# Kernel optimization log

Measured on AMD Instinct MI355X. Metric: run time of the kernel, lower is better.

Reference implementation:

```python
import jax, jax.numpy as jnp
import numpy as np

B, S, D, H, FF = 4, 1024, 1024, 16, 4096
DH = D // H
EPS = 1e-5


def setup_inputs() -> dict:
    key = jax.random.key(0)
    ks = jax.random.split(key, 24)
    w = lambda i, shp: jax.random.normal(ks[i], shp, jnp.float32) * 0.02
    inp = {
        'tgt': jax.random.normal(ks[0], (B, S, D), jnp.float32),
        'memory': jax.random.normal(ks[1], (B, S, D), jnp.float32),
        'mask': jax.random.randint(ks[2], (B, S, S), 0, 2, jnp.int32),
        # self-attention projections (stored [in,out]; torch Linear weight transposed)
        'sa_wq': w(3, (D, D)), 'sa_bq': jnp.zeros((D,), jnp.float32),
        'sa_wk': w(4, (D, D)), 'sa_bk': jnp.zeros((D,), jnp.float32),
        'sa_wv': w(5, (D, D)), 'sa_bv': jnp.zeros((D,), jnp.float32),
        'sa_wo': w(6, (D, D)), 'sa_bo': jnp.zeros((D,), jnp.float32),
        # cross-attention projections
        'ca_wq': w(7, (D, D)), 'ca_bq': jnp.zeros((D,), jnp.float32),
        'ca_wk': w(8, (D, D)), 'ca_bk': jnp.zeros((D,), jnp.float32),
        'ca_wv': w(9, (D, D)), 'ca_bv': jnp.zeros((D,), jnp.float32),
        'ca_wo': w(10, (D, D)), 'ca_bo': jnp.zeros((D,), jnp.float32),
        # FFN
        'w1': w(11, (D, FF)), 'b1': jnp.zeros((FF,), jnp.float32),
        'w2': w(12, (FF, D)), 'b2': jnp.zeros((D,), jnp.float32),
        # LayerNorms
        'g1': jnp.ones((D,), jnp.float32), 'be1': jnp.zeros((D,), jnp.float32),
        'g2': jnp.ones((D,), jnp.float32), 'be2': jnp.zeros((D,), jnp.float32),
        'g3': jnp.ones((D,), jnp.float32), 'be3': jnp.zeros((D,), jnp.float32),
    }
    return inp


def _layernorm(x, g, b):
    m = jnp.mean(x, axis=-1, keepdims=True)
    v = jnp.mean((x - m) ** 2, axis=-1, keepdims=True)
    return (x - m) * jax.lax.rsqrt(v + EPS) * g + b


def _mha(x, y, mask, wq, bq, wk, bk, wv, bv, wo, bo):
    # chunk(h,-1)+cat(0) head-split == reshape to [B,S,H,DH]
    b_, sq, _ = x.shape
    sk = y.shape[1]
    q = (x @ wq + bq).reshape(b_, sq, H, DH)
    k = (y @ wk + bk).reshape(b_, sk, H, DH)
    v = (y @ wv + bv).reshape(b_, sk, H, DH)
    score = jnp.einsum('bqhd,bkhd->bhqk', q, k) / jnp.float32(np.sqrt(DH))
    score = score + (1.0 - mask[:, None].astype(score.dtype)) * (-1e9)
    attn = jax.nn.softmax(score, axis=-1)
    out = jnp.einsum('bhqk,bkhd->bqhd', attn, v).reshape(b_, sq, D)
    return out @ wo + bo


def reference(tgt, memory, mask,
              sa_wq, sa_bq, sa_wk, sa_bk, sa_wv, sa_bv, sa_wo, sa_bo,
              ca_wq, ca_bq, ca_wk, ca_bk, ca_wv, ca_bv, ca_wo, ca_bo,
              w1, b1, w2, b2, g1, be1, g2, be2, g3, be3):
    t = tgt + _mha(tgt, tgt, mask, sa_wq, sa_bq, sa_wk, sa_bk, sa_wv, sa_bv, sa_wo, sa_bo)
    t = _layernorm(t, g1, be1)
    t = t + _mha(t, memory, mask, ca_wq, ca_bq, ca_wk, ca_bk, ca_wv, ca_bv, ca_wo, ca_bo)
    t = _layernorm(t, g2, be2)
    t = t + (jax.nn.relu(t @ w1 + b1) @ w2 + b2)
    t = _layernorm(t, g3, be3)
    return t
```

## Files before the change

kernel.cpp:

```cpp
#include <hip/hip_runtime.h>
#include <math.h>

typedef float f32x4 __attribute__((ext_vector_type(4)));
typedef unsigned short ushort8 __attribute__((ext_vector_type(8)));
typedef unsigned short ushort4v __attribute__((ext_vector_type(4)));
typedef __bf16 bf16x8 __attribute__((ext_vector_type(8)));
typedef unsigned int u32;

__device__ __forceinline__ unsigned short f2bf(float x) {
  union { float f; unsigned u; } v; v.f = x;
  unsigned r = v.u + 0x7FFFu + ((v.u >> 16) & 1u);
  return (unsigned short)(r >> 16);
}

__device__ __forceinline__ f32x4 mfma16(ushort8 a, ushort8 b, f32x4 c) {
  return __builtin_amdgcn_mfma_f32_16x16x32_bf16(
      __builtin_bit_cast(bf16x8, a), __builtin_bit_cast(bf16x8, b), c, 0, 0, 0);
}

__device__ __forceinline__ void gload16(const void* g, void* l) {
  __builtin_amdgcn_global_load_lds((const __attribute__((address_space(1))) u32*)g,
                                   (__attribute__((address_space(3))) u32*)l, 16, 0, 0);
}

__global__ __launch_bounds__(256) void gemm_bf16_kernel(
    const unsigned short* __restrict__ A, const unsigned short* __restrict__ Bt,
    const float* __restrict__ bias, void* __restrict__ C,
    int M, int N, int K, int flags)
{
  __shared__ __align__(16) char As0[128 * 128];
  __shared__ __align__(16) char Bs0[128 * 128];
  __shared__ __align__(16) char As1[128 * 128];
  __shared__ __align__(16) char Bs1[128 * 128];
  const int bn = blockIdx.x, bm = blockIdx.y;
  const int t = threadIdx.x;
  const int lane = t & 63, w = t >> 6, wm = w >> 1, wn = w & 1;
  const int l4 = lane & 15, lg = lane >> 4;
  const size_t K2 = (size_t)K * 2;

  f32x4 acc[4][4];
#pragma unroll
  for (int i = 0; i < 4; ++i)
#pragma unroll
    for (int j = 0; j < 4; ++j) acc[i][j] = f32x4{0.f, 0.f, 0.f, 0.f};

  const int lr = lane >> 3;
  const int ls = (lane & 7) ^ lr;
  const char* Ag = (const char*)A + (size_t)(bm * 128 + w * 32 + lr) * K2 + ls * 16;
  const char* Bg = (const char*)Bt + (size_t)(bn * 128 + w * 32 + lr) * K2 + ls * 16;
  const int wo = w * 4096;

  auto STAGE = [&](char* Al, char* Bl, int kt) {
    const size_t ko = (size_t)kt * 128;
#pragma unroll
    for (int i = 0; i < 4; ++i) {
      gload16(Ag + i * 8 * K2 + ko, Al + wo + i * 1024);
      gload16(Bg + i * 8 * K2 + ko, Bl + wo + i * 1024);
    }
  };
  auto COMPUTE = [&](const char* As, const char* Bs) {
#pragma unroll
    for (int ks = 0; ks < 2; ++ks) {
      const int kb = ks * 64 + lg * 16;
      ushort8 af[4], bfr[4];
#pragma unroll
      for (int mi = 0; mi < 4; ++mi) {
        int r = wm * 64 + mi * 16 + l4;
        af[mi] = *reinterpret_cast<const ushort8*>(As + r * 128 + (kb ^ ((r & 7) << 4)));
      }
#pragma unroll
      for (int ni = 0; ni < 4; ++ni) {
        int r = wn * 64 + ni * 16 + l4;
        bfr[ni] = *reinterpret_cast<const ushort8*>(Bs + r * 128 + (kb ^ ((r & 7) << 4)));
      }
#pragma unroll
      for (int mi = 0; mi < 4; ++mi)
#pragma unroll
        for (int ni = 0; ni < 4; ++ni)
          acc[mi][ni] = mfma16(af[mi], bfr[ni], acc[mi][ni]);
    }
  };

  const int nkt = K >> 6;
  STAGE(As0, Bs0, 0);
  __syncthreads();
  for (int kt = 0; kt < nkt; kt += 2) {
    STAGE(As1, Bs1, kt + 1);
    COMPUTE(As0, Bs0);
    __syncthreads();
    if (kt + 2 < nkt) STAGE(As0, Bs0, kt + 2);
    COMPUTE(As1, Bs1);
    __syncthreads();
  }

  const int relu = flags & 1, obf = flags & 2;
#pragma unroll
  for (int mi = 0; mi < 4; ++mi)
#pragma unroll
    for (int ni = 0; ni < 4; ++ni) {
      int col = bn * 128 + wn * 64 + ni * 16 + l4;
      float bia = bias[col];
#pragma unroll
      for (int j = 0; j < 4; ++j) {
        int row = bm * 128 + wm * 64 + mi * 16 + lg * 4 + j;
        float vv = acc[mi][ni][j] + bia;
        if (relu) vv = fmaxf(vv, 0.f);
        if (obf) ((unsigned short*)C)[(size_t)row * N + col] = f2bf(vv);
        else     ((float*)C)[(size_t)row * N + col] = vv;
      }
    }
}

constexpr int kS = 1024, kD = 1024, kDH = 64;

__global__ __launch_bounds__(256) void attn_kernel(
    const unsigned short* __restrict__ Qg, const unsigned short* __restrict__ Kg,
    const unsigned short* __restrict__ Vg, int qs, int ks_,
    const int* __restrict__ maskg, unsigned short* __restrict__ Og)
{
  __shared__ __align__(16) char Qs[64 * 128];
  __shared__ __align__(16) char Ks[64 * 128];
  __shared__ __align__(16) char VTs[64 * 128];
  __shared__ __align__(16) char Ps[4 * 16 * 128];
  const int qt = blockIdx.x, h = blockIdx.y, b = blockIdx.z;
  const int t = threadIdx.x, lane = t & 63, w = t >> 6;
  const int l4 = lane & 15, lg = lane >> 4;

  {
    int r = t >> 2, c0 = (t & 3) * 16;
    const unsigned short* src = Qg + (size_t)(b * kS + qt * 64 + r) * qs + h * kDH + c0;
#pragma unroll
    for (int hf = 0; hf < 2; ++hf) {
      ushort8 v = *reinterpret_cast<const ushort8*>(src + hf * 8);
      int c = c0 + hf * 8;
      *reinterpret_cast<ushort8*>(Qs + r * 128 + ((c * 2) ^ ((r & 7) << 4))) = v;
    }
  }

  float m_r[4], l_r[4];
  f32x4 o[4];
#pragma unroll
  for (int j = 0; j < 4; ++j) { m_r[j] = -1e30f; l_r[j] = 0.f; }
#pragma unroll
  for (int di = 0; di < 4; ++di) o[di] = f32x4{0.f, 0.f, 0.f, 0.f};

  for (int kt = 0; kt < kS / 64; ++kt) {
    __syncthreads();
    {
      int r = t >> 2, c0 = (t & 3) * 16;
      const unsigned short* src = Kg + (size_t)(b * kS + kt * 64 + r) * ks_ + h * kDH + c0;
#pragma unroll
      for (int hf = 0; hf < 2; ++hf) {
        ushort8 v = *reinterpret_cast<const ushort8*>(src + hf * 8);
        int c = c0 + hf * 8;
        *reinterpret_cast<ushort8*>(Ks + r * 128 + ((c * 2) ^ ((r & 7) << 4))) = v;
      }
    }
    {
      int key = t >> 2, c0 = (t & 3) * 16;
      const unsigned short* src = Vg + (size_t)(b * kS + kt * 64 + key) * ks_ + h * kDH + c0;
      ushort8 v0 = *reinterpret_cast<const ushort8*>(src);
      ushort8 v1 = *reinterpret_cast<const ushort8*>(src + 8);
#pragma unroll
      for (int i = 0; i < 16; ++i) {
        int dh = c0 + i;
        unsigned short vv = (i < 8) ? v0[i] : v1[i - 8];
        *reinterpret_cast<unsigned short*>(VTs + dh * 128 + ((key * 2) ^ ((dh & 7) << 4))) = vv;
      }
    }
    __syncthreads();

    f32x4 sc[4];
#pragma unroll
    for (int ni = 0; ni < 4; ++ni) sc[ni] = f32x4{0.f, 0.f, 0.f, 0.f};
#pragma unroll
    for (int ks = 0; ks < 2; ++ks) {
      const int kb = ks * 64 + lg * 16;
      int qr = w * 16 + l4;
      ushort8 a = *reinterpret_cast<const ushort8*>(Qs + qr * 128 + (kb ^ ((qr & 7) << 4)));
#pragma unroll
      for (int ni = 0; ni < 4; ++ni) {
        int kr = ni * 16 + l4;
        ushort8 bb = *reinterpret_cast<const ushort8*>(Ks + kr * 128 + (kb ^ ((kr & 7) << 4)));
        sc[ni] = mfma16(a, bb, sc[ni]);
      }
    }

    const int qbase = qt * 64 + w * 16;
    float pmax[4];
#pragma unroll
    for (int j = 0; j < 4; ++j) {
      int qrow = qbase + lg * 4 + j;
      const int* mrow = maskg + ((size_t)b * kS + qrow) * kS + kt * 64;
#pragma unroll
      for (int ni = 0; ni < 4; ++ni) {
        float mv = (float)mrow[ni * 16 + l4];
        sc[ni][j] = sc[ni][j] * 0.125f + (1.0f - mv) * (-1e9f);
      }
      pmax[j] = fmaxf(fmaxf(sc[0][j], sc[1][j]), fmaxf(sc[2][j], sc[3][j]));
    }
#pragma unroll
    for (int j = 0; j < 4; ++j)
#pragma unroll
      for (int off = 1; off < 16; off <<= 1)
        pmax[j] = fmaxf(pmax[j], __shfl_xor(pmax[j], off, 64));
    float alpha[4], rsum[4];
#pragma unroll
    for (int j = 0; j < 4; ++j) {
      float mn = fmaxf(m_r[j], pmax[j]);
      alpha[j] = __expf(m_r[j] - mn);
      m_r[j] = mn;
      rsum[j] = 0.f;
    }
#pragma unroll
    for (int ni = 0; ni < 4; ++ni)
#pragma unroll
      for (int j = 0; j < 4; ++j) {
        float p = __expf(sc[ni][j] - m_r[j]);
        sc[ni][j] = p;
        rsum[j] += p;
      }
#pragma unroll
    for (int j = 0; j < 4; ++j) {
#pragma unroll
      for (int off = 1; off < 16; off <<= 1)
        rsum[j] += __shfl_xor(rsum[j], off, 64);
      l_r[j] = l_r[j] * alpha[j] + rsum[j];
    }
#pragma unroll
    for (int di = 0; di < 4; ++di)
#pragma unroll
      for (int j = 0; j < 4; ++j) o[di][j] *= alpha[j];

    {
      char* Pw = Ps + w * 2048;
#pragma unroll
      for (int ni = 0; ni < 4; ++ni)
#pragma unroll
        for (int j = 0; j < 4; ++j) {
          int row = lg * 4 + j, col = ni * 16 + l4;
          *reinterpret_cast<unsigned short*>(Pw + row * 128 + ((col * 2) ^ ((row & 7) << 4))) = f2bf(sc[ni][j]);
        }
    }
    __syncthreads();
    {
      const char* Pw = Ps + w * 2048;
#pragma unroll
      for (int ks = 0; ks < 2; ++ks) {
        const int kb = ks * 64 + lg * 16;
        ushort8 pa = *reinterpret_cast<const ushort8*>(Pw + l4 * 128 + (kb ^ ((l4 & 7) << 4)));
#pragma unroll
        for (int di = 0; di < 4; ++di) {
          int vr = di * 16 + l4;
          ushort8 vb = *reinterpret_cast<const ushort8*>(VTs + vr * 128 + (kb ^ ((vr & 7) << 4)));
          o[di] = mfma16(pa, vb, o[di]);
        }
      }
    }
  }

#pragma unroll
  for (int di = 0; di < 4; ++di) {
    int col = h * kDH + di * 16 + l4;
#pragma unroll
    for (int j = 0; j < 4; ++j) {
      int qrow = qt * 64 + w * 16 + lg * 4 + j;
      Og[(size_t)(b * kS + qrow) * kD + col] = f2bf(o[di][j] / l_r[j]);
    }
  }
}

__global__ __launch_bounds__(256) void addln_kernel(
    const float* __restrict__ x, const float* __restrict__ y,
    const float* __restrict__ g, const float* __restrict__ be,
    float* __restrict__ out, unsigned short* __restrict__ ob)
{
  const int row = blockIdx.x, t = threadIdx.x;
  const size_t base = (size_t)row * 1024 + t * 4;
  float4 xv = *reinterpret_cast<const float4*>(x + base);
  float4 yv = *reinterpret_cast<const float4*>(y + base);
  float v0 = xv.x + yv.x, v1 = xv.y + yv.y, v2 = xv.z + yv.z, v3 = xv.w + yv.w;
  float s1 = v0 + v1 + v2 + v3;
  float s2 = v0 * v0 + v1 * v1 + v2 * v2 + v3 * v3;
#pragma unroll
  for (int off = 1; off < 64; off <<= 1) {
    s1 += __shfl_xor(s1, off, 64);
    s2 += __shfl_xor(s2, off, 64);
  }
  __shared__ float r1[4], r2[4];
  const int w = t >> 6, lane = t & 63;
  if (lane == 0) { r1[w] = s1; r2[w] = s2; }
  __syncthreads();
  s1 = r1[0] + r1[1] + r1[2] + r1[3];
  s2 = r2[0] + r2[1] + r2[2] + r2[3];
  const float mean = s1 * (1.0f / 1024.0f);
  const float var = s2 * (1.0f / 1024.0f) - mean * mean;
  const float rs = rsqrtf(var + 1e-5f);
  float4 gv = *reinterpret_cast<const float4*>(g + t * 4);
  float4 bv = *reinterpret_cast<const float4*>(be + t * 4);
  float4 ov;
  ov.x = (v0 - mean) * rs * gv.x + bv.x;
  ov.y = (v1 - mean) * rs * gv.y + bv.y;
  ov.z = (v2 - mean) * rs * gv.z + bv.z;
  ov.w = (v3 - mean) * rs * gv.w + bv.w;
  *reinterpret_cast<float4*>(out + base) = ov;
  if (ob) {
    ushort4v bo;
    bo[0] = f2bf(ov.x); bo[1] = f2bf(ov.y); bo[2] = f2bf(ov.z); bo[3] = f2bf(ov.w);
    *reinterpret_cast<ushort4v*>(ob + base) = bo;
  }
}

__global__ __launch_bounds__(256) void cvt2_bf16_kernel(
    const float* __restrict__ a, const float* __restrict__ b,
    unsigned short* __restrict__ da, unsigned short* __restrict__ db, int n8each)
{
  int i = blockIdx.x * 256 + threadIdx.x;
  const float* s = a; unsigned short* d = da;
  if (i >= n8each) { s = b; d = db; i -= n8each; }
  if (i >= n8each) return;
  float4 f0 = reinterpret_cast<const float4*>(s)[i * 2];
  float4 f1 = reinterpret_cast<const float4*>(s)[i * 2 + 1];
  ushort8 v;
  v[0] = f2bf(f0.x); v[1] = f2bf(f0.y); v[2] = f2bf(f0.z); v[3] = f2bf(f0.w);
  v[4] = f2bf(f1.x); v[5] = f2bf(f1.y); v[6] = f2bf(f1.z); v[7] = f2bf(f1.w);
  reinterpret_cast<ushort8*>(d)[i] = v;
}

__global__ __launch_bounds__(256) void transpose_cvt_kernel(
    const float* __restrict__ src, unsigned short* __restrict__ dst, int K, int N)
{
  __shared__ float tile[32][33];
  const int bx = blockIdx.x, by = blockIdx.y;
  const int tx = threadIdx.x & 31, ty = threadIdx.x >> 5;
#pragma unroll
  for (int i = 0; i < 4; ++i)
    tile[ty + i * 8][tx] = src[(size_t)(by * 32 + ty + i * 8) * N + bx * 32 + tx];
  __syncthreads();
#pragma unroll
  for (int i = 0; i < 4; ++i)
    dst[(size_t)(bx * 32 + ty + i * 8) * K + by * 32 + tx] = f2bf(tile[tx][ty + i * 8]);
}

struct TPtrs { const float* s[8]; unsigned short* d[8]; };
__global__ __launch_bounds__(256) void tcvt_batch_kernel(TPtrs p)
{
  __shared__ float tile[32][33];
  const float* __restrict__ src = p.s[blockIdx.z];
  unsigned short* __restrict__ dst = p.d[blockIdx.z];
  const int bx = blockIdx.x, by = blockIdx.y;
  const int tx = threadIdx.x & 31, ty = threadIdx.x >> 5;
#pragma unroll
  for (int i = 0; i < 4; ++i)
    tile[ty + i * 8][tx] = src[(size_t)(by * 32 + ty + i * 8) * 1024 + bx * 32 + tx];
  __syncthreads();
#pragma unroll
  for (int i = 0; i < 4; ++i)
    dst[(size_t)(bx * 32 + ty + i * 8) * 1024 + by * 32 + tx] = f2bf(tile[tx][ty + i * 8]);
}

__global__ void biasprep_kernel(const float* sq, const float* sk, const float* sv,
                                const float* ck, const float* cv,
                                float* bsa, float* bca)
{
  int i = blockIdx.x * 256 + threadIdx.x;
  if (i < 3072) bsa[i] = (i < 1024) ? sq[i] : (i < 2048 ? sk[i - 1024] : sv[i - 2048]);
  int j = i - 3072;
  if (j >= 0 && j < 2048) bca[j] = (j < 1024) ? ck[j] : cv[j - 1024];
}

extern "C" void kernel_launch(void* const* d_in, const int* in_sizes, int n_in,
                              void* d_out, int out_size, void* d_ws, size_t ws_size,
                              hipStream_t stream)
{
  const float* tgt  = (const float*)d_in[0];
  const float* memi = (const float*)d_in[1];
  const int*   mask = (const int*)d_in[2];
  const float* sa_wq = (const float*)d_in[3];  const float* sa_bq = (const float*)d_in[4];
  const float* sa_wk = (const float*)d_in[5];  const float* sa_bk = (const float*)d_in[6];
  const float* sa_wv = (const float*)d_in[7];  const float* sa_bv = (const float*)d_in[8];
  const float* sa_wo = (const float*)d_in[9];  const float* sa_bo = (const float*)d_in[10];
  const float* ca_wq = (const float*)d_in[11]; const float* ca_bq = (const float*)d_in[12];
  const float* ca_wk = (const float*)d_in[13]; const float* ca_bk = (const float*)d_in[14];
  const float* ca_wv = (const float*)d_in[15]; const float* ca_bv = (const float*)d_in[16];
  const float* ca_wo = (const float*)d_in[17]; const float* ca_bo = (const float*)d_in[18];
  const float* w1 = (const float*)d_in[19]; const float* b1 = (const float*)d_in[20];
  const float* w2 = (const float*)d_in[21]; const float* b2 = (const float*)d_in[22];
  const float* g1 = (const float*)d_in[23]; const float* be1 = (const float*)d_in[24];
  const float* g2 = (const float*)d_in[25]; const float* be2 = (const float*)d_in[26];
  const float* g3 = (const float*)d_in[27]; const float* be3 = (const float*)d_in[28];
  float* out = (float*)d_out;
  char* W = (char*)d_ws;
  const size_t MB = 1 << 20;
  typedef unsigned short us;

  us* Wsaqkv = (us*)(W + 0);
  us* Wsao   = (us*)(W + 6 * MB);
  us* Wcaq   = (us*)(W + 8 * MB);
  us* Wcakv  = (us*)(W + 10 * MB);
  us* Wcao   = (us*)(W + 14 * MB);
  us* W1t    = (us*)(W + 16 * MB);
  us* W2t    = (us*)(W + 24 * MB);
  float* b_saqkv = (float*)(W + 32 * MB);
  float* b_cakv  = (float*)(W + 32 * MB + 16384);
  us* tgt_bf = (us*)(W + 33 * MB);
  us* T2b    = tgt_bf;
  us* mem_bf = (us*)(W + 41 * MB);
  us* QKV    = (us*)(W + 49 * MB);
  us* Qca    = (us*)(W + 49 * MB);
  us* KVca   = (us*)(W + 57 * MB);
  us* T1b    = (us*)(W + 65 * MB);
  us* AO     = (us*)(W + 73 * MB);
  us* Hb     = (us*)(W + 49 * MB);
  float* Op  = (float*)(W + 81 * MB);
  float* T1f = (float*)(W + 97 * MB);
  float* T2f = T1f;

  const int M = 4096;
  dim3 blk(256);
  auto gemm = [&](const us* Aa, const us* Bta, const float* bias, void* Cc,
                  int Nn, int Kk, int flags) {
    gemm_bf16_kernel<<<dim3(Nn / 128, M / 128), blk, 0, stream>>>(Aa, Bta, bias, Cc, M, Nn, Kk, flags);
  };

  TPtrs tp;
  tp.s[0] = sa_wq; tp.d[0] = Wsaqkv;
  tp.s[1] = sa_wk; tp.d[1] = Wsaqkv + 1024 * 1024;
  tp.s[2] = sa_wv; tp.d[2] = Wsaqkv + 2048 * 1024;
  tp.s[3] = sa_wo; tp.d[3] = Wsao;
  tp.s[4] = ca_wq; tp.d[4] = Wcaq;
  tp.s[5] = ca_wk; tp.d[5] = Wcakv;
  tp.s[6] = ca_wv; tp.d[6] = Wcakv + 1024 * 1024;
  tp.s[7] = ca_wo; tp.d[7] = Wcao;
  tcvt_batch_kernel<<<dim3(32, 32, 8), blk, 0, stream>>>(tp);
  transpose_cvt_kernel<<<dim3(128, 32), blk, 0, stream>>>(w1, W1t, 1024, 4096);
  transpose_cvt_kernel<<<dim3(32, 128), blk, 0, stream>>>(w2, W2t, 4096, 1024);
  cvt2_bf16_kernel<<<dim3(4096), blk, 0, stream>>>(tgt, memi, tgt_bf, mem_bf, M * 1024 / 8);
  biasprep_kernel<<<dim3(20), blk, 0, stream>>>(sa_bq, sa_bk, sa_bv, ca_bk, ca_bv, b_saqkv, b_cakv);

  gemm(tgt_bf, Wsaqkv, b_saqkv, QKV, 3072, 1024, 2);
  attn_kernel<<<dim3(16, 16, 4), blk, 0, stream>>>(QKV, QKV + 1024, QKV + 2048, 3072, 3072, mask, AO);
  gemm(AO, Wsao, sa_bo, Op, 1024, 1024, 0);
  addln_kernel<<<dim3(M), blk, 0, stream>>>(tgt, Op, g1, be1, T1f, T1b);

  gemm(T1b, Wcaq, ca_bq, Qca, 1024, 1024, 2);
  gemm(mem_bf, Wcakv, b_cakv, KVca, 2048, 1024, 2);
  attn_kernel<<<dim3(16, 16, 4), blk, 0, stream>>>(Qca, KVca, KVca + 1024, 1024, 2048, mask, AO);
  gemm(AO, Wcao, ca_bo, Op, 1024, 1024, 0);
  addln_kernel<<<dim3(M), blk, 0, stream>>>(T1f, Op, g2, be2, T2f, T2b);

  gemm(T2b, W1t, b1, Hb, 4096, 1024, 3);
  gemm(Hb, W2t, b2, Op, 1024, 4096, 0);
  addln_kernel<<<dim3(M), blk, 0, stream>>>(T2f, Op, g3, be3, out, nullptr);

  (void)in_sizes; (void)n_in; (void)out_size; (void)ws_size; (void)mask;
}
```

Baseline: 445.9 us.

## Pipeline attention with async K/mask staging, bf16 mask bias, folded scale, bf16 residuals

Rewrites the attention kernel to double-buffer K, V and mask tiles, using direct global-to-LDS loads so the next tile is fetched while the current one is computed. The int32 mask is precomputed once into a swizzled bf16 additive bias. The 1/sqrt(d)*log2(e) factor is folded into the Q weights and biases so softmax can use exp2. The running max is only rescaled when it grows past a threshold. Separately, the output-projection GEMMs now write bf16 instead of fp32 for the add+LayerNorm kernels, cutting memory traffic at some precision cost.

```diff
diff --git a/kernel.cpp b/kernel.cpp
--- a/kernel.cpp
+++ b/kernel.cpp
@@ -11,6 +11,9 @@
   union { float f; unsigned u; } v; v.f = x;
   unsigned r = v.u + 0x7FFFu + ((v.u >> 16) & 1u);
   return (unsigned short)(r >> 16);
+}
+__device__ __forceinline__ float bf2f(unsigned short u) {
+  union { unsigned u; float f; } c; c.u = ((unsigned)u) << 16; return c.f;
 }
 
 __device__ __forceinline__ f32x4 mfma16(ushort8 a, ushort8 b, f32x4 c) {
@@ -116,15 +119,20 @@
 __global__ __launch_bounds__(256) void attn_kernel(
     const unsigned short* __restrict__ Qg, const unsigned short* __restrict__ Kg,
     const unsigned short* __restrict__ Vg, int qs, int ks_,
-    const int* __restrict__ maskg, unsigned short* __restrict__ Og)
-{
-  __shared__ __align__(16) char Qs[64 * 128];
-  __shared__ __align__(16) char Ks[64 * 128];
-  __shared__ __align__(16) char VTs[64 * 128];
-  __shared__ __align__(16) char Ps[4 * 16 * 128];
+    const unsigned short* __restrict__ mbias, unsigned short* __restrict__ Og)
+{
+  __shared__ __align__(16) char Qs[8192];
+  __shared__ __align__(16) char Ks0[8192];
+  __shared__ __align__(16) char Ks1[8192];
+  __shared__ __align__(16) char Ms0[8192];
+  __shared__ __align__(16) char Ms1[8192];
+  __shared__ __align__(16) char VT0[8192];
+  __shared__ __align__(16) char VT1[8192];
+  __shared__ __align__(16) char Ps[8192];
   const int qt = blockIdx.x, h = blockIdx.y, b = blockIdx.z;
   const int t = threadIdx.x, lane = t & 63, w = t >> 6;
   const int l4 = lane & 15, lg = lane >> 4;
+  const int lr = lane >> 3, sg = (lane & 7) ^ lr;
 
   {
     int r = t >> 2, c0 = (t & 3) * 16;
@@ -137,6 +145,18 @@
     }
   }
 
+  auto stageK = [&](char* Kl, int kt) {
+    const char* base = (const char*)(Kg + (size_t)(b * kS + kt * 64) * ks_ + h * kDH) + sg * 16;
+    gload16(base + (size_t)(w * 16 + lr) * (ks_ * 2), Kl + w * 2048);
+    gload16(base + (size_t)(w * 16 + 8 + lr) * (ks_ * 2), Kl + w * 2048 + 1024);
+  };
+  auto stageM = [&](char* Ml, int kt) {
+    const char* base = (const char*)mbias + ((size_t)(b * 1024 + qt * 64) * 1024 + kt * 64) * 2
+                       + (lane & 7) * 16;
+    gload16(base + (size_t)(w * 16 + lr) * 2048, Ml + w * 2048);
+    gload16(base + (size_t)(w * 16 + 8 + lr) * 2048, Ml + w * 2048 + 1024);
+  };
+
   float m_r[4], l_r[4];
   f32x4 o[4];
 #pragma unroll
@@ -144,142 +164,175 @@
 #pragma unroll
   for (int di = 0; di < 4; ++di) o[di] = f32x4{0.f, 0.f, 0.f, 0.f};
 
-  for (int kt = 0; kt < kS / 64; ++kt) {
-    __syncthreads();
-    {
-      int r = t >> 2, c0 = (t & 3) * 16;
-      const unsigned short* src = Kg + (size_t)(b * kS + kt * 64 + r) * ks_ + h * kDH + c0;
-#pragma unroll
-      for (int hf = 0; hf < 2; ++hf) {
-        ushort8 v = *reinterpret_cast<const ushort8*>(src + hf * 8);
-        int c = c0 + hf * 8;
-        *reinterpret_cast<ushort8*>(Ks + r * 128 + ((c * 2) ^ ((r & 7) << 4))) = v;
-      }
-    }
-    {
-      int key = t >> 2, c0 = (t & 3) * 16;
-      const unsigned short* src = Vg + (size_t)(b * kS + kt * 64 + key) * ks_ + h * kDH + c0;
-      ushort8 v0 = *reinterpret_cast<const ushort8*>(src);
-      ushort8 v1 = *reinterpret_cast<const ushort8*>(src + 8);
-#pragma unroll
-      for (int i = 0; i < 16; ++i) {
-        int dh = c0 + i;
-        unsigned short vv = (i < 8) ? v0[i] : v1[i - 8];
-        *reinterpret_cast<unsigned short*>(VTs + dh * 128 + ((key * 2) ^ ((dh & 7) << 4))) = vv;
-      }
-    }
-    __syncthreads();
-
-    f32x4 sc[4];
-#pragma unroll
-    for (int ni = 0; ni < 4; ++ni) sc[ni] = f32x4{0.f, 0.f, 0.f, 0.f};
-#pragma unroll
-    for (int ks = 0; ks < 2; ++ks) {
-      const int kb = ks * 64 + lg * 16;
-      int qr = w * 16 + l4;
-      ushort8 a = *reinterpret_cast<const ushort8*>(Qs + qr * 128 + (kb ^ ((qr & 7) << 4)));
-#pragma unroll
-      for (int ni = 0; ni < 4; ++ni) {
-        int kr = ni * 16 + l4;
-        ushort8 bb = *reinterpret_cast<const ushort8*>(Ks + kr * 128 + (kb ^ ((kr & 7) << 4)));
-        sc[ni] = mfma16(a, bb, sc[ni]);
-      }
-    }
-
-    const int qbase = qt * 64 + w * 16;
-    float pmax[4];
-#pragma unroll
-    for (int j = 0; j < 4; ++j) {
-      int qrow = qbase + lg * 4 + j;
-      const int* mrow = maskg + ((size_t)b * kS + qrow) * kS + kt * 64;
-#pragma unroll
-      for (int ni = 0; ni < 4; ++ni) {
-        float mv = (float)mrow[ni * 16 + l4];
-        sc[ni][j] = sc[ni][j] * 0.125f + (1.0f - mv) * (-1e9f);
-      }
-      pmax[j] = fmaxf(fmaxf(sc[0][j], sc[1][j]), fmaxf(sc[2][j], sc[3][j]));
-    }
-#pragma unroll
-    for (int j = 0; j < 4; ++j)
-#pragma unroll
-      for (int off = 1; off < 16; off <<= 1)
-        pmax[j] = fmaxf(pmax[j], __shfl_xor(pmax[j], off, 64));
-    float alpha[4], rsum[4];
-#pragma unroll
-    for (int j = 0; j < 4; ++j) {
-      float mn = fmaxf(m_r[j], pmax[j]);
-      alpha[j] = __expf(m_r[j] - mn);
-      m_r[j] = mn;
-      rsum[j] = 0.f;
-    }
-#pragma unroll
-    for (int ni = 0; ni < 4; ++ni)
-#pragma unroll
-      for (int j = 0; j < 4; ++j) {
-        float p = __expf(sc[ni][j] - m_r[j]);
-        sc[ni][j] = p;
-        rsum[j] += p;
-      }
-#pragma unroll
-    for (int j = 0; j < 4; ++j) {
-#pragma unroll
-      for (int off = 1; off < 16; off <<= 1)
-        rsum[j] += __shfl_xor(rsum[j], off, 64);
-      l_r[j] = l_r[j] * alpha[j] + rsum[j];
-    }
-#pragma unroll
-    for (int di = 0; di < 4; ++di)
-#pragma unroll
-      for (int j = 0; j < 4; ++j) o[di][j] *= alpha[j];
-
-    {
-      char* Pw = Ps + w * 2048;
-#pragma unroll
-      for (int ni = 0; ni < 4; ++ni)
-#pragma unroll
-        for (int j = 0; j < 4; ++j) {
-          int row = lg * 4 + j, col = ni * 16 + l4;
-          *reinterpret_cast<unsigned short*>(Pw + row * 128 + ((col * 2) ^ ((row & 7) << 4))) = f2bf(sc[ni][j]);
-        }
-    }
-    __syncthreads();
-    {
-      const char* Pw = Ps + w * 2048;
-#pragma unroll
-      for (int ks = 0; ks < 2; ++ks) {
-        const int kb = ks * 64 + lg * 16;
-        ushort8 pa = *reinterpret_cast<const ushort8*>(Pw + l4 * 128 + (kb ^ ((l4 & 7) << 4)));
-#pragma unroll
-        for (int di = 0; di < 4; ++di) {
-          int vr = di * 16 + l4;
-          ushort8 vb = *reinterpret_cast<const ushort8*>(VTs + vr * 128 + (kb ^ ((vr & 7) << 4)));
-          o[di] = mfma16(pa, vb, o[di]);
-        }
-      }
-    }
-  }
-
+  ushort8 vA0, vA1, vB0, vB1;
+  stageK(Ks0, 0);
+  stageM(Ms0, 0);
+  {
+    const unsigned short* vsrc = Vg + (size_t)(b * kS + (t >> 2)) * ks_ + h * kDH + (t & 3) * 16;
+    vA0 = *reinterpret_cast<const ushort8*>(vsrc);
+    vA1 = *reinterpret_cast<const ushort8*>(vsrc + 8);
+  }
+
+#define ATTN_TILE(KC, MC, VC, KN, MN, VC0, VC1, VN0, VN1, KTV)                           \
+  {                                                                                      \
+    asm volatile("s_waitcnt vmcnt(0)" ::: "memory");                                     \
+    __builtin_amdgcn_s_barrier();                                                        \
+    __builtin_amdgcn_sched_barrier(0);                                                   \
+    {                                      \
+      int key2 = (t >> 2) * 2, c0 = (t & 3) * 16;                                        \
+      _Pragma("unroll")                                                                  \
+      for (int i = 0; i < 8; ++i) {                                                      \
+        int dh = c0 + i;                                                                 \
+        *(unsigned short*)(VC + dh * 128 +                                               \
+            (key2 ^ ((dh & 7) << 4) ^ ((dh >> 4) << 5))) = VC0[i];                       \
+      }                                                                                  \
+      _Pragma("unroll")                                                                  \
+      for (int i = 0; i < 8; ++i) {                                                      \
+        int dh = c0 + 8 + i;                                                             \
+        *(unsigned short*)(VC + dh * 128 +                                               \
+            (key2 ^ ((dh & 7) << 4) ^ ((dh >> 4) << 5))) = VC1[i];                       \
+      }                                                                                  \
+    }                                                                                    \
+    if ((KTV) + 1 < 16) {                  \
+      stageK(KN, (KTV) + 1);                                                             \
+      stageM(MN, (KTV) + 1);                                                             \
+      const unsigned short* vsrc = Vg +                                                  \
+          (size_t)(b * kS + ((KTV) + 1) * 64 + (t >> 2)) * ks_ + h * kDH + (t & 3) * 16; \
+      VN0 = *reinterpret_cast<const ushort8*>(vsrc);                                     \
+      VN1 = *reinterpret_cast<const ushort8*>(vsrc + 8);                                 \
+    }                                                                                    \
+    f32x4 sc[4];                                                                         \
+    _Pragma("unroll")                                                                    \
+    for (int ni = 0; ni < 4; ++ni) sc[ni] = f32x4{0.f, 0.f, 0.f, 0.f};                   \
+    __builtin_amdgcn_s_setprio(1);                                                       \
+    _Pragma("unroll")                                                                    \
+    for (int ks = 0; ks < 2; ++ks) {                                                     \
+      const int kb = ks * 64 + lg * 16;                                                  \
+      int qr = w * 16 + l4;                                                              \
+      ushort8 a = *(const ushort8*)(Qs + qr * 128 + (kb ^ ((qr & 7) << 4)));             \
+      _Pragma("unroll")                                                                  \
+      for (int ni = 0; ni < 4; ++ni) {                                                   \
+        int kr = ni * 16 + l4;                                                           \
+        ushort8 bb = *(const ushort8*)(KC + kr * 128 + (kb ^ ((kr & 7) << 4)));          \
+        sc[ni] = mfma16(a, bb, sc[ni]);                                                  \
+      }                                                                                  \
+    }                                                                                    \
+    __builtin_amdgcn_s_setprio(0);                                                       \
+    float pmax[4];                                                                       \
+    _Pragma("unroll")                                                                    \
+    for (int j = 0; j < 4; ++j) {                                                        \
+      int row = lg * 4 + j;                                                              \
+      _Pragma("unroll")                                                                  \
+      for (int ni = 0; ni < 4; ++ni) {                                                   \
+        int col = ni * 16 + l4;                                                          \
+        unsigned short mu = *(const unsigned short*)(MC + w * 2048 + row * 128 +         \
+            ((col * 2) ^ ((row & 7) << 4) ^ ((row & 8) << 2)));                          \
+        sc[ni][j] += bf2f(mu);                                                           \
+      }                                                                                  \
+      pmax[j] = fmaxf(fmaxf(sc[0][j], sc[1][j]), fmaxf(sc[2][j], sc[3][j]));             \
+    }                                                                                    \
+    _Pragma("unroll")                                                                    \
+    for (int j = 0; j < 4; ++j) {                                                        \
+      pmax[j] = fmaxf(pmax[j], __shfl_xor(pmax[j], 1, 64));                              \
+      pmax[j] = fmaxf(pmax[j], __shfl_xor(pmax[j], 2, 64));                              \
+      pmax[j] = fmaxf(pmax[j], __shfl_xor(pmax[j], 4, 64));                              \
+      pmax[j] = fmaxf(pmax[j], __shfl_xor(pmax[j], 8, 64));                              \
+    }                                                                                    \
+    bool need = (pmax[0] > m_r[0] + 8.f) || (pmax[1] > m_r[1] + 8.f) ||                  \
+                (pmax[2] > m_r[2] + 8.f) || (pmax[3] > m_r[3] + 8.f);                    \
+    if (__any(need)) {                                                                   \
+      _Pragma("unroll")                                                                  \
+      for (int j = 0; j < 4; ++j) {                                                      \
+        float mn = fmaxf(m_r[j], pmax[j]);                                               \
+        float al = exp2f(m_r[j] - mn);                                                   \
+        m_r[j] = mn; l_r[j] *= al;                                                       \
+        o[0][j] *= al; o[1][j] *= al; o[2][j] *= al; o[3][j] *= al;                      \
+      }                                                                                  \
+    }                                                                                    \
+    float rsum[4] = {0.f, 0.f, 0.f, 0.f};                                                \
+    _Pragma("unroll")                                                                    \
+    for (int ni = 0; ni < 4; ++ni)                                                       \
+      _Pragma("unroll")                                                                  \
+      for (int j = 0; j < 4; ++j) {                                                      \
+        float p = exp2f(sc[ni][j] - m_r[j]);                                             \
+        sc[ni][j] = p;                                                                   \
+        rsum[j] += p;                                                                    \
+      }                                                                                  \
+    _Pragma("unroll")                                                                    \
+    for (int j = 0; j < 4; ++j) {                                                        \
+      rsum[j] += __shfl_xor(rsum[j], 1, 64);                                             \
+      rsum[j] += __shfl_xor(rsum[j], 2, 64);                                             \
+      rsum[j] += __shfl_xor(rsum[j], 4, 64);                                             \
+      rsum[j] += __shfl_xor(rsum[j], 8, 64);                                             \
+      l_r[j] += rsum[j];                                                                 \
+    }                                                                                    \
+    {                               \
+      char* Pw = Ps + w * 2048;                                                          \
+      _Pragma("unroll")                                                                  \
+      for (int ni = 0; ni < 4; ++ni)                                                     \
+        _Pragma("unroll")                                                                \
+        for (int j = 0; j < 4; ++j) {                                                    \
+          int row = lg * 4 + j, col = ni * 16 + l4;                                      \
+          *(unsigned short*)(Pw + row * 128 +                                            \
+              ((col * 2) ^ ((row & 7) << 4) ^ ((row & 8) << 2))) =                       \
+              __builtin_bit_cast(unsigned short, (__bf16)sc[ni][j]);                     \
+        }                                                                                \
+    }                                                                                    \
+    asm volatile("s_waitcnt lgkmcnt(0)" ::: "memory");                                   \
+    __builtin_amdgcn_s_barrier();                                                        \
+    __builtin_amdgcn_sched_barrier(0);                                                   \
+    __builtin_amdgcn_s_setprio(1);                                                       \
+    {                                                                                    \
+      const char* Pw = Ps + w * 2048;                                                    \
+      _Pragma("unroll")                                                                  \
+      for (int ks = 0; ks < 2; ++ks) {                                                   \
+        const int kb = ks * 64 + lg * 16;                                                \
+        ushort8 pa = *(const ushort8*)(Pw + l4 * 128 +                                   \
+            (kb ^ ((l4 & 7) << 4) ^ ((l4 & 8) << 2)));                                   \
+        _Pragma("unroll")                                                                \
+        for (int di = 0; di < 4; ++di) {                                                 \
+          int vr2 = di * 16 + l4;                                                        \
+          ushort8 vb = *(const ushort8*)(VC + vr2 * 128 +                                \
+              (kb ^ ((vr2 & 7) << 4) ^ ((vr2 >> 4) << 5)));                              \
+          o[di] = mfma16(pa, vb, o[di]);                                                 \
+        }                                                                                \
+      }                                                                                  \
+    }                                                                                    \
+    __builtin_amdgcn_s_setprio(0);                                                       \
+  }
+
+  for (int kt = 0; kt < 16; kt += 2) {
+    ATTN_TILE(Ks0, Ms0, VT0, Ks1, Ms1, vA0, vA1, vB0, vB1, kt);
+    ATTN_TILE(Ks1, Ms1, VT1, Ks0, Ms0, vB0, vB1, vA0, vA1, kt + 1);
+  }
+#undef ATTN_TILE
+
+  float rinv[4];
+#pragma unroll
+  for (int j = 0; j < 4; ++j) rinv[j] = 1.0f / l_r[j];
 #pragma unroll
   for (int di = 0; di < 4; ++di) {
     int col = h * kDH + di * 16 + l4;
 #pragma unroll
     for (int j = 0; j < 4; ++j) {
       int qrow = qt * 64 + w * 16 + lg * 4 + j;
-      Og[(size_t)(b * kS + qrow) * kD + col] = f2bf(o[di][j] / l_r[j]);
+      Og[(size_t)(b * kS + qrow) * kD + col] =
+          __builtin_bit_cast(unsigned short, (__bf16)(o[di][j] * rinv[j]));
     }
   }
 }
 
 __global__ __launch_bounds__(256) void addln_kernel(
-    const float* __restrict__ x, const float* __restrict__ y,
+    const float* __restrict__ x, const unsigned short* __restrict__ y,
     const float* __restrict__ g, const float* __restrict__ be,
     float* __restrict__ out, unsigned short* __restrict__ ob)
 {
   const int row = blockIdx.x, t = threadIdx.x;
   const size_t base = (size_t)row * 1024 + t * 4;
   float4 xv = *reinterpret_cast<const float4*>(x + base);
-  float4 yv = *reinterpret_cast<const float4*>(y + base);
-  float v0 = xv.x + yv.x, v1 = xv.y + yv.y, v2 = xv.z + yv.z, v3 = xv.w + yv.w;
+  ushort4v yv = *reinterpret_cast<const ushort4v*>(y + base);
+  float v0 = xv.x + bf2f(yv[0]), v1 = xv.y + bf2f(yv[1]);
+  float v2 = xv.z + bf2f(yv[2]), v3 = xv.w + bf2f(yv[3]);
   float s1 = v0 + v1 + v2 + v3;
   float s2 = v0 * v0 + v1 * v1 + v2 * v2 + v3 * v3;
 #pragma unroll
@@ -342,12 +395,13 @@
     dst[(size_t)(bx * 32 + ty + i * 8) * K + by * 32 + tx] = f2bf(tile[tx][ty + i * 8]);
 }
 
-struct TPtrs { const float* s[8]; unsigned short* d[8]; };
+struct TPtrs { const float* s[8]; unsigned short* d[8]; float scale[8]; };
 __global__ __launch_bounds__(256) void tcvt_batch_kernel(TPtrs p)
 {
   __shared__ float tile[32][33];
   const float* __restrict__ src = p.s[blockIdx.z];
   unsigned short* __restrict__ dst = p.d[blockIdx.z];
+  const float sc = p.scale[blockIdx.z];
   const int bx = blockIdx.x, by = blockIdx.y;
   const int tx = threadIdx.x & 31, ty = threadIdx.x >> 5;
 #pragma unroll
@@ -356,17 +410,36 @@
   __syncthreads();
 #pragma unroll
   for (int i = 0; i < 4; ++i)
-    dst[(size_t)(bx * 32 + ty + i * 8) * 1024 + by * 32 + tx] = f2bf(tile[tx][ty + i * 8]);
+    dst[(size_t)(bx * 32 + ty + i * 8) * 1024 + by * 32 + tx] = f2bf(tile[tx][ty + i * 8] * sc);
 }
 
 __global__ void biasprep_kernel(const float* sq, const float* sk, const float* sv,
-                                const float* ck, const float* cv,
-                                float* bsa, float* bca)
+                                const float* cq, const float* ck, const float* cv,
+                                float* bsa, float* bca, float* bcq, float s)
 {
   int i = blockIdx.x * 256 + threadIdx.x;
-  if (i < 3072) bsa[i] = (i < 1024) ? sq[i] : (i < 2048 ? sk[i - 1024] : sv[i - 2048]);
-  int j = i - 3072;
-  if (j >= 0 && j < 2048) bca[j] = (j < 1024) ? ck[j] : cv[j - 1024];
+  if (i < 1024) { bsa[i] = sq[i] * s; bcq[i] = cq[i] * s; bca[i] = ck[i]; bca[i + 1024] = cv[i]; }
+  else if (i < 2048) bsa[i] = sk[i - 1024];
+  else if (i < 3072) bsa[i] = sv[i - 2048];
+}
+
+__global__ __launch_bounds__(256) void maskprep_kernel(
+    const int* __restrict__ mask, unsigned short* __restrict__ mbias)
+{
+  int idx = blockIdx.x * 256 + threadIdx.x;
+  int chunk = idx & 127;
+  int q = (idx >> 7) & 1023;
+  int b = idx >> 17;
+  int tile = chunk >> 3, slot = chunk & 7;
+  int sslot = slot ^ (q & 7) ^ ((q & 8) >> 2);
+  const int* src = mask + ((size_t)(b * 1024 + q) * 1024) + tile * 64 + sslot * 8;
+  int4 m0 = *reinterpret_cast<const int4*>(src);
+  int4 m1 = *reinterpret_cast<const int4*>(src + 4);
+  const unsigned short NEG = 0xCE6E;
+  ushort8 v;
+  v[0] = m0.x ? 0 : NEG; v[1] = m0.y ? 0 : NEG; v[2] = m0.z ? 0 : NEG; v[3] = m0.w ? 0 : NEG;
+  v[4] = m1.x ? 0 : NEG; v[5] = m1.y ? 0 : NEG; v[6] = m1.z ? 0 : NEG; v[7] = m1.w ? 0 : NEG;
+  *reinterpret_cast<ushort8*>(mbias + (size_t)idx * 8) = v;
 }
 
 extern "C" void kernel_launch(void* const* d_in, const int* in_sizes, int n_in,
@@ -393,6 +466,7 @@
   char* W = (char*)d_ws;
   const size_t MB = 1 << 20;
   typedef unsigned short us;
+  const float QSCALE = 0.18033688011112042f;
 
   us* Wsaqkv = (us*)(W + 0);
   us* Wsao   = (us*)(W + 6 * MB);
@@ -403,6 +477,7 @@
   us* W2t    = (us*)(W + 24 * MB);
   float* b_saqkv = (float*)(W + 32 * MB);
   float* b_cakv  = (float*)(W + 32 * MB + 16384);
+  float* b_caq   = (float*)(W + 32 * MB + 32768);
   us* tgt_bf = (us*)(W + 33 * MB);
   us* T2b    = tgt_bf;
   us* mem_bf = (us*)(W + 41 * MB);
@@ -412,8 +487,9 @@
   us* T1b    = (us*)(W + 65 * MB);
   us* AO     = (us*)(W + 73 * MB);
   us* Hb     = (us*)(W + 49 * MB);
-  float* Op  = (float*)(W + 81 * MB);
-  float* T1f = (float*)(W + 97 * MB);
+  us* Opb    = (us*)(W + 81 * MB);
+  us* mbias  = (us*)(W + 89 * MB);
+  float* T1f = (float*)(W + 98 * MB);
   float* T2f = T1f;
 
   const int M = 4096;
@@ -424,34 +500,36 @@
   };
 
   TPtrs tp;
-  tp.s[0] = sa_wq; tp.d[0] = Wsaqkv;
-  tp.s[1] = sa_wk; tp.d[1] = Wsaqkv + 1024 * 1024;
-  tp.s[2] = sa_wv; tp.d[2] = Wsaqkv + 2048 * 1024;
-  tp.s[3] = sa_wo; tp.d[3] = Wsao;
-  tp.s[4] = ca_wq; tp.d[4] = Wcaq;
-  tp.s[5] = ca_wk; tp.d[5] = Wcakv;
-  tp.s[6] = ca_wv; tp.d[6] = Wcakv + 1024 * 1024;
-  tp.s[7] = ca_wo; tp.d[7] = Wcao;
+  tp.s[0] = sa_wq; tp.d[0] = Wsaqkv;              tp.scale[0] = QSCALE;
+  tp.s[1] = sa_wk; tp.d[1] = Wsaqkv + 1024 * 1024; tp.scale[1] = 1.f;
+  tp.s[2] = sa_wv; tp.d[2] = Wsaqkv + 2048 * 1024; tp.scale[2] = 1.f;
+  tp.s[3] = sa_wo; tp.d[3] = Wsao;                 tp.scale[3] = 1.f;
+  tp.s[4] = ca_wq; tp.d[4] = Wcaq;                 tp.scale[4] = QSCALE;
+  tp.s[5] = ca_wk; tp.d[5] = Wcakv;                tp.scale[5] = 1.f;
+  tp.s[6] = ca_wv; tp.d[6] = Wcakv + 1024 * 1024;  tp.scale[6] = 1.f;
+  tp.s[7] = ca_wo; tp.d[7] = Wcao;                 tp.scale[7] = 1.f;
   tcvt_batch_kernel<<<dim3(32, 32, 8), blk, 0, stream>>>(tp);
   transpose_cvt_kernel<<<dim3(128, 32), blk, 0, stream>>>(w1, W1t, 1024, 4096);
   transpose_cvt_kernel<<<dim3(32, 128), blk, 0, stream>>>(w2, W2t, 4096, 1024);
   cvt2_bf16_kernel<<<dim3(4096), blk, 0, stream>>>(tgt, memi, tgt_bf, mem_bf, M * 1024 / 8);
-  biasprep_kernel<<<dim3(20), blk, 0, stream>>>(sa_bq, sa_bk, sa_bv, ca_bk, ca_bv, b_saqkv, b_cakv);
+  biasprep_kernel<<<dim3(12), blk, 0, stream>>>(sa_bq, sa_bk, sa_bv, ca_bq, ca_bk, ca_bv,
+                                                b_saqkv, b_cakv, b_caq, QSCALE);
+  maskprep_kernel<<<dim3(2048), blk, 0, stream>>>(mask, mbias);
 
   gemm(tgt_bf, Wsaqkv, b_saqkv, QKV, 3072, 1024, 2);
-  attn_kernel<<<dim3(16, 16, 4), blk, 0, stream>>>(QKV, QKV + 1024, QKV + 2048, 3072, 3072, mask, AO);
-  gemm(AO, Wsao, sa_bo, Op, 1024, 1024, 0);
-  addln_kernel<<<dim3(M), blk, 0, stream>>>(tgt, Op, g1, be1, T1f, T1b);
-
-  gemm(T1b, Wcaq, ca_bq, Qca, 1024, 1024, 2);
+  attn_kernel<<<dim3(16, 16, 4), blk, 0, stream>>>(QKV, QKV + 1024, QKV + 2048, 3072, 3072, mbias, AO);
+  gemm(AO, Wsao, sa_bo, Opb, 1024, 1024, 2);
+  addln_kernel<<<dim3(M), blk, 0, stream>>>(tgt, Opb, g1, be1, T1f, T1b);
+
+  gemm(T1b, Wcaq, b_caq, Qca, 1024, 1024, 2);
   gemm(mem_bf, Wcakv, b_cakv, KVca, 2048, 1024, 2);
-  attn_kernel<<<dim3(16, 16, 4), blk, 0, stream>>>(Qca, KVca, KVca + 1024, 1024, 2048, mask, AO);
-  gemm(AO, Wcao, ca_bo, Op, 1024, 1024, 0);
-  addln_kernel<<<dim3(M), blk, 0, stream>>>(T1f, Op, g2, be2, T2f, T2b);
+  attn_kernel<<<dim3(16, 16, 4), blk, 0, stream>>>(Qca, KVca, KVca + 1024, 1024, 2048, mbias, AO);
+  gemm(AO, Wcao, ca_bo, Opb, 1024, 1024, 2);
+  addln_kernel<<<dim3(M), blk, 0, stream>>>(T1f, Opb, g2, be2, T2f, T2b);
 
   gemm(T2b, W1t, b1, Hb, 4096, 1024, 3);
-  gemm(Hb, W2t, b2, Op, 1024, 4096, 0);
-  addln_kernel<<<dim3(M), blk, 0, stream>>>(T2f, Op, g3, be3, out, nullptr);
-
-  (void)in_sizes; (void)n_in; (void)out_size; (void)ws_size; (void)mask;
-}
+  gemm(Hb, W2t, b2, Opb, 1024, 4096, 2);
+  addln_kernel<<<dim3(M), blk, 0, stream>>>(T2f, Opb, g3, be3, out, nullptr);
+
+  (void)in_sizes; (void)n_in; (void)out_size; (void)ws_size;
+}
```

Measured after the change: 464.9 us. +4.3%, slower.
